# Optimization experiments

Hardware: AMD Instinct MI355X
Metric: run time of the kernel (lower is better)

## Reference

```python
import jax, jax.numpy as jnp
import numpy as np

N_HEADS = 16

def setup_inputs() -> dict:
    key = jax.random.key(0)
    ks = jax.random.split(key, 7)
    B, T, C = 2, 2048, 1024
    s = 0.02  # weight init scale
    return {
        "x": jax.random.normal(ks[0], (B, T, C), jnp.float32),
        "attention_mask": jnp.ones((B, T), jnp.float32),
        "Wq": jax.random.normal(ks[1], (C, C), jnp.float32) * s,
        "Wk": jax.random.normal(ks[2], (C, C), jnp.float32) * s,
        "Wv": jax.random.normal(ks[3], (C, C), jnp.float32) * s,
        "Wp": jax.random.normal(ks[4], (C, C), jnp.float32) * s,
        "bp": jax.random.normal(ks[5], (C,), jnp.float32) * s,
    }

def reference(x, attention_mask, Wq, Wk, Wv, Wp, bp):
    B, T, C = x.shape
    H = N_HEADS
    d = C // H
    q = (x @ Wq).reshape(B, T, H, d)
    k = (x @ Wk).reshape(B, T, H, d)
    v = (x @ Wv).reshape(B, T, H, d)
    # scores scaled by C**-0.5 (embedding dim), as in the source
    wei = jnp.einsum('bihd,bjhd->bhij', q, k) * (C ** -0.5)
    causal = jnp.tril(jnp.ones((T, T), bool))  # tril buffer, T == block_size
    wei = jnp.where(causal[None, None], wei, -jnp.inf)
    wei = jax.nn.softmax(wei, axis=-1)
    # NOTE: source's post-softmax padding masked_fill is not in-place -> no-op.
    # Dropout in eval mode -> identity.
    out = jnp.einsum('bhij,bjhd->bihd', wei, v).reshape(B, T, C)
    return out @ Wp + bp
```

## Files before the change

### kernel.cpp

```cpp
#include <hip/hip_runtime.h>
#include <hip/hip_bf16.h>
#include <stdint.h>

#define BB 2
#define TT 2048
#define CC 1024
#define HH 16
#define DD 64
#define MM (BB*TT)

#define C2SCALE 0.045084220027780106f

typedef __bf16 bf16x8 __attribute__((ext_vector_type(8)));
typedef float f32x4 __attribute__((ext_vector_type(4)));

__device__ __forceinline__ void load_lds16(const void* g, void* l) {
    __builtin_amdgcn_global_load_lds((const __attribute__((address_space(1))) uint32_t*)g,
                                     (__attribute__((address_space(3))) uint32_t*)l,
                                     16, 0, 0);
}

__global__ __launch_bounds__(256)
void conv_bf16(const float* __restrict__ in, __hip_bfloat16* __restrict__ out, int n4) {
    int i = blockIdx.x * 256 + threadIdx.x;
    if (i >= n4) return;
    float4 f = reinterpret_cast<const float4*>(in)[i];
    union { __hip_bfloat16 h[4]; uint2 u; } cv;
    cv.h[0] = __float2bfloat16(f.x);
    cv.h[1] = __float2bfloat16(f.y);
    cv.h[2] = __float2bfloat16(f.z);
    cv.h[3] = __float2bfloat16(f.w);
    reinterpret_cast<uint2*>(out)[i] = cv.u;
}

__global__ __launch_bounds__(256)
void transpose_conv4(const float* __restrict__ W0, const float* __restrict__ W1,
                     const float* __restrict__ W2, const float* __restrict__ W3,
                     __hip_bfloat16* __restrict__ out) {
    __shared__ float t[32][33];
    const int z = blockIdx.z;
    const float* W = (z == 0) ? W0 : (z == 1) ? W1 : (z == 2) ? W2 : W3;
    __hip_bfloat16* Wt = out + (size_t)z * CC * CC;
    int kt = blockIdx.x * 32, nt = blockIdx.y * 32;
    int tx = threadIdx.x & 31, ty = threadIdx.x >> 5;
#pragma unroll
    for (int r = 0; r < 32; r += 8)
        t[ty + r][tx] = W[(size_t)(kt + ty + r) * CC + nt + tx];
    __syncthreads();
#pragma unroll
    for (int r = 0; r < 32; r += 8)
        Wt[(size_t)(nt + ty + r) * CC + kt + tx] = __float2bfloat16(t[tx][ty + r]);
}

template <int MODE>
__global__ __launch_bounds__(256)
void gemm_bt(const __hip_bfloat16* __restrict__ A,
             const __hip_bfloat16* __restrict__ Bt,
             void* __restrict__ out0, void* __restrict__ out1, void* __restrict__ out2,
             const float* __restrict__ bias,
             int M, int N, int K) {
    __shared__ __hip_bfloat16 As[2][128 * 64];
    __shared__ __hip_bfloat16 Bs[2][128 * 64];

    const int tid = threadIdx.x;
    const int wave = tid >> 6, lane = tid & 63;
    const int lg = lane >> 4, lr = lane & 15;
    const int wm = wave >> 1, wn = wave & 1;
    const int bm0 = blockIdx.y * 128, bn0 = blockIdx.x * 128;

    auto stage = [&](int slot, int k0) {
#pragma unroll
        for (int it = 0; it < 4; ++it) {
            int c = it * 256 + tid;
            int row = c >> 3, sub = c & 7;
            int g = sub ^ (row & 7);
            load_lds16((const char*)(A + (size_t)(bm0 + row) * K + k0) + g * 16,
                       (char*)As[slot] + c * 16);
        }
#pragma unroll
        for (int it = 0; it < 4; ++it) {
            int c = it * 256 + tid;
            int row = c >> 3, sub = c & 7;
            int g = sub ^ (row & 7);
            load_lds16((const char*)(Bt + (size_t)(bn0 + row) * K + k0) + g * 16,
                       (char*)Bs[slot] + c * 16);
        }
    };

    f32x4 acc[4][4] = {};

    auto compute = [&](int slot) {
        const char* as = (const char*)As[slot];
        const char* bs = (const char*)Bs[slot];
        bf16x8 af[2][4], bf[2][4];
#pragma unroll
        for (int kk = 0; kk < 2; ++kk) {
#pragma unroll
            for (int m = 0; m < 4; ++m) {
                int row = wm * 64 + m * 16 + lr;
                af[kk][m] = *(const bf16x8*)(as + row * 128 + (((kk * 4 + lg) ^ (row & 7)) * 16));
            }
#pragma unroll
            for (int n = 0; n < 4; ++n) {
                int row = wn * 64 + n * 16 + lr;
                bf[kk][n] = *(const bf16x8*)(bs + row * 128 + (((kk * 4 + lg) ^ (row & 7)) * 16));
            }
        }
#pragma unroll
        for (int kk = 0; kk < 2; ++kk)
#pragma unroll
            for (int m = 0; m < 4; ++m)
#pragma unroll
                for (int n = 0; n < 4; ++n)
                    acc[m][n] = __builtin_amdgcn_mfma_f32_16x16x32_bf16(af[kk][m], bf[kk][n], acc[m][n], 0, 0, 0);
    };

    const int NT = K >> 6;
    stage(0, 0);
    for (int t = 0; t < NT; ++t) {
        __syncthreads();
        if (t + 1 < NT) stage((t + 1) & 1, (t + 1) * 64);
        compute(t & 1);
    }

#pragma unroll
    for (int m = 0; m < 4; ++m)
#pragma unroll
        for (int n = 0; n < 4; ++n) {
            int row0 = bm0 + wm * 64 + m * 16 + lg * 4;
            int colf = bn0 + wn * 64 + n * 16 + lr;
            if (MODE == 2) {
#pragma unroll
                for (int r = 0; r < 4; ++r)
                    ((float*)out0)[(size_t)(row0 + r) * N + colf] = acc[m][n][r] + bias[colf];
            } else {
                int which = colf >> 10, col = colf & 1023;
                if (which < 2) {
                    __hip_bfloat16* o = which ? (__hip_bfloat16*)out1 : (__hip_bfloat16*)out0;
                    float sc = which ? 1.0f : C2SCALE;
#pragma unroll
                    for (int r = 0; r < 4; ++r)
                        o[(size_t)(row0 + r) * 1024 + col] = __float2bfloat16(acc[m][n][r] * sc);
                } else {
                    int hh = col >> 6, dd = col & 63;
                    int bI = row0 >> 11, tt = row0 & 2047;
                    union { __hip_bfloat16 h[4]; uint2 u; } pk;
#pragma unroll
                    for (int r = 0; r < 4; ++r) pk.h[r] = __float2bfloat16(acc[m][n][r]);
                    *(uint2*)((__hip_bfloat16*)out2 + ((size_t)(bI * HH + hh) * DD + dd) * TT + tt) = pk.u;
                }
            }
        }
}

__global__ __launch_bounds__(512)
void attn_kernel(const __hip_bfloat16* __restrict__ Q,
                 const __hip_bfloat16* __restrict__ K,
                 const __hip_bfloat16* __restrict__ Vt,
                 __hip_bfloat16* __restrict__ att) {
    __shared__ __hip_bfloat16 Ks[2][64 * 64];
    __shared__ __hip_bfloat16 Vs[2][64 * 64];
    __shared__ __hip_bfloat16 Pl[8][16 * 72];

    const int tid = threadIdx.x;
    const int wave = tid >> 6, lane = tid & 63;
    const int lg = lane >> 4, lr = lane & 15;

    int id = blockIdx.x;
    int rest = id >> 3;
    int qt = rest & 15;
    int hb = (id & 7) + ((rest >> 4) << 3);
    const int h = hb & 15, b = hb >> 4;
    if (b & 1) qt = 15 - qt;

    const size_t baseQK = ((size_t)b * TT) * CC + (size_t)h * DD;
    const __hip_bfloat16* Vth = Vt + ((size_t)(b * HH + h)) * DD * TT;
    const int wq0 = qt * 128 + wave * 16;

    bf16x8 qf[2];
#pragma unroll
    for (int kf = 0; kf < 2; ++kf)
        qf[kf] = *(const bf16x8*)&Q[baseQK + (size_t)(wq0 + lr) * CC + kf * 32 + lg * 8];

    float m_run = -1e30f, l_run = 0.f;
    f32x4 o[4] = {};

    const int nkt = qt * 2 + 2;

    auto stage = [&](int bufi, int kv0) {
        int row = tid >> 3, sub = tid & 7;
        int g = sub ^ (row & 7);
        load_lds16((const char*)(K + baseQK + (size_t)(kv0 + row) * CC) + g * 16,
                   (char*)Ks[bufi] + tid * 16);
        load_lds16((const char*)(Vth + (size_t)row * TT + kv0) + g * 16,
                   (char*)Vs[bufi] + tid * 16);
    };

    stage(0, 0);

    for (int kt = 0; kt < nkt; ++kt) {
        const int kv0 = kt * 64;
        __syncthreads();
        if (kt + 1 < nkt) stage((kt + 1) & 1, kv0 + 64);
        const char* Kb = (const char*)Ks[kt & 1];
        const char* Vb = (const char*)Vs[kt & 1];

        if (kv0 > wq0 + 15) continue;

        f32x4 s[4] = {};
#pragma unroll
        for (int kf = 0; kf < 2; ++kf) {
            bf16x8 kfr[4];
#pragma unroll
            for (int nf = 0; nf < 4; ++nf)
                kfr[nf] = *(const bf16x8*)(Kb + (nf * 16 + lr) * 128 + (((kf * 4 + lg) ^ (lr & 7)) * 16));
#pragma unroll
            for (int nf = 0; nf < 4; ++nf)
                s[nf] = __builtin_amdgcn_mfma_f32_16x16x32_bf16(kfr[nf], qf[kf], s[nf], 0, 0, 0);
        }

        const bool needMask = (kv0 + 63 > wq0);
        const int qg = wq0 + lr;
        float mx = -1e30f;
#pragma unroll
        for (int nf = 0; nf < 4; ++nf)
#pragma unroll
            for (int r = 0; r < 4; ++r) {
                float sv = s[nf][r];
                if (needMask) {
                    int kvg = kv0 + nf * 16 + lg * 4 + r;
                    sv = (kvg > qg) ? -1e30f : sv;
                    s[nf][r] = sv;
                }
                mx = fmaxf(mx, sv);
            }
        mx = fmaxf(mx, __shfl_xor(mx, 16, 64));
        mx = fmaxf(mx, __shfl_xor(mx, 32, 64));

        bool grow = __any(mx > m_run + 8.0f);
        float sc = 0.0f;
        if (grow) {
            float mnew = fmaxf(m_run, mx);
            sc = __builtin_amdgcn_exp2f(m_run - mnew);
            m_run = mnew;
        }
        float rsum = 0.f;
#pragma unroll
        for (int nf = 0; nf < 4; ++nf)
#pragma unroll
            for (int r = 0; r < 4; ++r) {
                float p = __builtin_amdgcn_exp2f(s[nf][r] - m_run);
                s[nf][r] = p;
                rsum += p;
            }
        rsum += __shfl_xor(rsum, 16, 64);
        rsum += __shfl_xor(rsum, 32, 64);
        if (grow) {
            l_run = l_run * sc + rsum;
#pragma unroll
            for (int r = 0; r < 4; ++r) {
                float sco = __shfl(sc, lg * 4 + r, 64);
#pragma unroll
                for (int df = 0; df < 4; ++df) o[df][r] *= sco;
            }
        } else {
            l_run += rsum;
        }

        __hip_bfloat16* Pw = &Pl[wave][0];
#pragma unroll
        for (int nf = 0; nf < 4; ++nf) {
            union { __hip_bfloat16 h[4]; uint2 u; } pk;
#pragma unroll
            for (int r = 0; r < 4; ++r) pk.h[r] = __float2bfloat16(s[nf][r]);
            *(uint2*)&Pw[lr * 72 + nf * 16 + lg * 4] = pk.u;
        }

#pragma unroll
        for (int ks = 0; ks < 2; ++ks) {
            bf16x8 pf = *(const bf16x8*)&Pw[lr * 72 + ks * 32 + lg * 8];
            bf16x8 vf[4];
#pragma unroll
            for (int df = 0; df < 4; ++df)
                vf[df] = *(const bf16x8*)(Vb + (df * 16 + lr) * 128 + (((ks * 4 + lg) ^ (lr & 7)) * 16));
#pragma unroll
            for (int df = 0; df < 4; ++df)
                o[df] = __builtin_amdgcn_mfma_f32_16x16x32_bf16(pf, vf[df], o[df], 0, 0, 0);
        }
    }

#pragma unroll
    for (int r = 0; r < 4; ++r) {
        float lo = __shfl(l_run, lg * 4 + r, 64);
        float inv = 1.0f / lo;
        int qg = wq0 + lg * 4 + r;
#pragma unroll
        for (int df = 0; df < 4; ++df)
            att[baseQK + (size_t)qg * CC + df * 16 + lr] = __float2bfloat16(o[df][r] * inv);
    }
}

extern "C" void kernel_launch(void* const* d_in, const int* in_sizes, int n_in,
                              void* d_out, int out_size, void* d_ws, size_t ws_size,
                              hipStream_t stream) {
    const float* x  = (const float*)d_in[0];
    const float* Wq = (const float*)d_in[2];
    const float* Wk = (const float*)d_in[3];
    const float* Wv = (const float*)d_in[4];
    const float* Wp = (const float*)d_in[5];
    const float* bp = (const float*)d_in[6];
    float* out = (float*)d_out;

    __hip_bfloat16* ws  = (__hip_bfloat16*)d_ws;
    __hip_bfloat16* xb  = ws;
    __hip_bfloat16* wqt = xb  + (size_t)MM * CC;
    __hip_bfloat16* wpt = wqt + 3 * (size_t)CC * CC;
    __hip_bfloat16* Qb  = wpt + (size_t)CC * CC;
    __hip_bfloat16* Kb  = Qb  + (size_t)MM * CC;
    __hip_bfloat16* VtG = Kb  + (size_t)MM * CC;
    __hip_bfloat16* att = VtG + (size_t)MM * CC;

    conv_bf16<<<(MM * CC / 4 + 255) / 256, 256, 0, stream>>>(x, xb, MM * CC / 4);
    transpose_conv4<<<dim3(CC / 32, CC / 32, 4), 256, 0, stream>>>(Wq, Wk, Wv, Wp, wqt);

    dim3 gq(3 * CC / 128, MM / 128);
    gemm_bt<1><<<gq, 256, 0, stream>>>(xb, wqt, Qb, Kb, VtG, nullptr, MM, 3 * CC, CC);

    attn_kernel<<<dim3(512), 512, 0, stream>>>(Qb, Kb, VtG, att);

    dim3 gp(CC / 128, MM / 128);
    gemm_bt<2><<<gp, 256, 0, stream>>>(att, wpt, out, nullptr, nullptr, bp, MM, CC, CC);
}
```

Baseline: 200.8 us.

## Make GEMM waves stage private LDS tiles and drop block barriers

Each wave now loads its own 64-row A and B slices into a private LDS region with a new swizzle, and the K step drops to 32. Block-wide __syncthreads is replaced by explicit vmcnt waits. This removes barrier stalls between waves, at the cost of loading each A and B slice twice across waves, which raises global/L2 traffic.

```diff
diff --git a/kernel.cpp b/kernel.cpp
--- a/kernel.cpp
+++ b/kernel.cpp
@@ -59,8 +59,7 @@
              void* __restrict__ out0, void* __restrict__ out1, void* __restrict__ out2,
              const float* __restrict__ bias,
              int M, int N, int K) {
-    __shared__ __hip_bfloat16 As[2][128 * 64];
-    __shared__ __hip_bfloat16 Bs[2][128 * 64];
+    __shared__ char lds[4][2][8192];
 
     const int tid = threadIdx.x;
     const int wave = tid >> 6, lane = tid & 63;
@@ -68,58 +67,57 @@
     const int wm = wave >> 1, wn = wave & 1;
     const int bm0 = blockIdx.y * 128, bn0 = blockIdx.x * 128;
 
+    const __hip_bfloat16* Aw = A + (size_t)(bm0 + wm * 64) * K;
+    const __hip_bfloat16* Bw = Bt + (size_t)(bn0 + wn * 64) * K;
+
     auto stage = [&](int slot, int k0) {
-#pragma unroll
-        for (int it = 0; it < 4; ++it) {
-            int c = it * 256 + tid;
-            int row = c >> 3, sub = c & 7;
-            int g = sub ^ (row & 7);
-            load_lds16((const char*)(A + (size_t)(bm0 + row) * K + k0) + g * 16,
-                       (char*)As[slot] + c * 16);
-        }
-#pragma unroll
-        for (int it = 0; it < 4; ++it) {
-            int c = it * 256 + tid;
-            int row = c >> 3, sub = c & 7;
-            int g = sub ^ (row & 7);
-            load_lds16((const char*)(Bt + (size_t)(bn0 + row) * K + k0) + g * 16,
-                       (char*)Bs[slot] + c * 16);
+        char* base = lds[wave][slot];
+#pragma unroll
+        for (int i = 0; i < 4; ++i) {
+            int c = lane + 64 * i;
+            int row = c >> 2, p = c & 3;
+            int g = p ^ ((row >> 1) & 3);
+            load_lds16((const char*)(Aw + (size_t)row * K + k0) + g * 16, base + c * 16);
+        }
+#pragma unroll
+        for (int i = 0; i < 4; ++i) {
+            int c = lane + 64 * i;
+            int row = c >> 2, p = c & 3;
+            int g = p ^ ((row >> 1) & 3);
+            load_lds16((const char*)(Bw + (size_t)row * K + k0) + g * 16, base + 4096 + c * 16);
         }
     };
 
     f32x4 acc[4][4] = {};
+    const int rchunk = lg ^ ((lr >> 1) & 3);
 
     auto compute = [&](int slot) {
-        const char* as = (const char*)As[slot];
-        const char* bs = (const char*)Bs[slot];
-        bf16x8 af[2][4], bf[2][4];
-#pragma unroll
-        for (int kk = 0; kk < 2; ++kk) {
-#pragma unroll
-            for (int m = 0; m < 4; ++m) {
-                int row = wm * 64 + m * 16 + lr;
-                af[kk][m] = *(const bf16x8*)(as + row * 128 + (((kk * 4 + lg) ^ (row & 7)) * 16));
-            }
-#pragma unroll
-            for (int n = 0; n < 4; ++n) {
-                int row = wn * 64 + n * 16 + lr;
-                bf[kk][n] = *(const bf16x8*)(bs + row * 128 + (((kk * 4 + lg) ^ (row & 7)) * 16));
-            }
-        }
-#pragma unroll
-        for (int kk = 0; kk < 2; ++kk)
-#pragma unroll
-            for (int m = 0; m < 4; ++m)
-#pragma unroll
-                for (int n = 0; n < 4; ++n)
-                    acc[m][n] = __builtin_amdgcn_mfma_f32_16x16x32_bf16(af[kk][m], bf[kk][n], acc[m][n], 0, 0, 0);
+        const char* as = lds[wave][slot];
+        const char* bs = as + 4096;
+        bf16x8 af[4], bf[4];
+#pragma unroll
+        for (int m = 0; m < 4; ++m)
+            af[m] = *(const bf16x8*)(as + (m * 16 + lr) * 64 + rchunk * 16);
+#pragma unroll
+        for (int n = 0; n < 4; ++n)
+            bf[n] = *(const bf16x8*)(bs + (n * 16 + lr) * 64 + rchunk * 16);
+#pragma unroll
+        for (int m = 0; m < 4; ++m)
+#pragma unroll
+            for (int n = 0; n < 4; ++n)
+                acc[m][n] = __builtin_amdgcn_mfma_f32_16x16x32_bf16(af[m], bf[n], acc[m][n], 0, 0, 0);
     };
 
-    const int NT = K >> 6;
+    const int NT = K >> 5;
     stage(0, 0);
+    __builtin_amdgcn_sched_barrier(0);
     for (int t = 0; t < NT; ++t) {
-        __syncthreads();
-        if (t + 1 < NT) stage((t + 1) & 1, (t + 1) * 64);
+        if (t + 1 < NT) {
+            stage((t + 1) & 1, (t + 1) * 32);
+            asm volatile("s_waitcnt vmcnt(8)" ::: "memory");
+        } else {
+            asm volatile("s_waitcnt vmcnt(0)" ::: "memory");
+        }
         compute(t & 1);
     }
 
```

After: 196.9 us. About the same (-1.9%).
